# Kernel tuning notes

Hardware: AMD Instinct MI355X
Metric: run time of the kernel (lower is better)

## Reference

```python
import jax, jax.numpy as jnp
import numpy as np

INPUT_SIZE = 256
N_DIM = 128
BATCH = 1024


def setup_inputs() -> dict:
    key = jax.random.key(0)
    ks = jax.random.split(key, 8)
    X = jax.random.normal(ks[0], (BATCH, INPUT_SIZE), dtype=jnp.float32)
    h = jax.random.normal(ks[1], (BATCH, INPUT_SIZE * N_DIM), dtype=jnp.float32)
    W_r = jax.random.normal(ks[2], (INPUT_SIZE, 1, N_DIM), dtype=jnp.float32)
    W_z = jax.random.normal(ks[3], (INPUT_SIZE, 1, N_DIM), dtype=jnp.float32)
    W_h = jax.random.normal(ks[4], (INPUT_SIZE, 1, N_DIM), dtype=jnp.float32)
    # orthogonal init for U (matches nn.init.orthogonal_ in spirit)
    def ortho(k):
        a = jax.random.normal(k, (INPUT_SIZE, N_DIM, N_DIM), dtype=jnp.float32)
        q, _ = jnp.linalg.qr(a)
        return q.astype(jnp.float32)
    U_r = ortho(ks[5])
    U_z = ortho(ks[6])
    U_h = ortho(ks[7])
    b_r = jnp.zeros((INPUT_SIZE, N_DIM), dtype=jnp.float32)
    b_z = jnp.zeros((INPUT_SIZE, N_DIM), dtype=jnp.float32)
    b_h = jnp.zeros((INPUT_SIZE, N_DIM), dtype=jnp.float32)
    return {"X": X, "h": h, "W_r": W_r, "W_z": W_z, "W_h": W_h,
            "U_r": U_r, "U_z": U_z, "U_h": U_h,
            "b_r": b_r, "b_z": b_z, "b_h": b_h}


def reference(X, h, W_r, W_z, W_h, U_r, U_z, U_h, b_r, b_z, b_h):
    B = X.shape[0]
    hg = h.reshape(B, INPUT_SIZE, N_DIM)  # [B, I, D]
    # X contribution: X[b,i] * W[i,0,k] -> [B, I, D]
    xW_r = X[:, :, None] * W_r[:, 0, :][None]
    xW_z = X[:, :, None] * W_z[:, 0, :][None]
    xW_h = X[:, :, None] * W_h[:, 0, :][None]
    # grouped GEMMs: [B,I,D] x [I,D,D] -> [B,I,D]
    r = jax.nn.sigmoid(xW_r + jnp.einsum('bij,ijk->bik', hg, U_r) + b_r)
    z = jax.nn.sigmoid(xW_z + jnp.einsum('bij,ijk->bik', hg, U_z) + b_z)
    h_tilde = jnp.tanh(xW_h + jnp.einsum('bij,ijk->bik', r * hg, U_h) + b_h)
    h_new = z * hg + (1.0 - z) * h_tilde
    return (h_new.reshape(B, INPUT_SIZE * N_DIM),
            h_tilde.reshape(B, INPUT_SIZE * N_DIM))
```

## Files before the change

### kernel.cpp

```cpp
#include <hip/hip_runtime.h>
#include <stdint.h>

#define I_SIZE 256
#define D_DIM 128
#define BATCH 1024
#define S_LDS 136
#define THREADS 512
#define CHUNKS 2
#define ROWS_PER_CHUNK (BATCH / CHUNKS)
#define ROWS_PER_PASS 128
#define PASSES (ROWS_PER_CHUNK / ROWS_PER_PASS)

typedef __attribute__((ext_vector_type(8))) short short8;
typedef __attribute__((ext_vector_type(4))) short short4v;
typedef __attribute__((ext_vector_type(4))) float floatx4;

__device__ inline short f2bf(float f) {
    union { float f; uint32_t u; } v; v.f = f;
    uint32_t u = v.u;
    uint32_t r = (u + 0x7FFFu + ((u >> 16) & 1u)) >> 16;
    return (short)(r & 0xFFFFu);
}
__device__ inline float bf2f(short s) {
    union { uint32_t u; float f; } v; v.u = ((uint32_t)(uint16_t)s) << 16;
    return v.f;
}
__device__ inline float sigmoidf_fast(float x) { return 1.0f / (1.0f + __expf(-x)); }
__device__ inline float tanhf_fast(float x)    { return 2.0f / (1.0f + __expf(-2.0f * x)) - 1.0f; }

__global__ __launch_bounds__(THREADS, 2) void gru_kernel(
    const float* __restrict__ X, const float* __restrict__ H,
    const float* __restrict__ Wr, const float* __restrict__ Wz, const float* __restrict__ Wh,
    const float* __restrict__ Ur, const float* __restrict__ Uz, const float* __restrict__ Uh,
    const float* __restrict__ br, const float* __restrict__ bz, const float* __restrict__ bh,
    float* __restrict__ out)
{
    __shared__ short Ut[3][D_DIM * S_LDS];
    __shared__ short hgb[ROWS_PER_PASS * S_LDS];
    __shared__ float Wl[6][D_DIM];

    const int tid   = threadIdx.x;
    const int group = blockIdx.x & 255;
    const int chunk = blockIdx.x >> 8;
    const int batch0 = chunk * ROWS_PER_CHUNK;

    if (tid < D_DIM) {
        Wl[0][tid] = Wr[group * D_DIM + tid];
        Wl[1][tid] = Wz[group * D_DIM + tid];
        Wl[2][tid] = Wh[group * D_DIM + tid];
        Wl[3][tid] = br[group * D_DIM + tid];
        Wl[4][tid] = bz[group * D_DIM + tid];
        Wl[5][tid] = bh[group * D_DIM + tid];
    }

    {
        const int jj = tid >> 5;
        const int k0 = (tid & 31) * 4;
        const float* Us0 = Ur + (size_t)group * (D_DIM * D_DIM);
        const float* Us1 = Uz + (size_t)group * (D_DIM * D_DIM);
        const float* Us2 = Uh + (size_t)group * (D_DIM * D_DIM);
        #pragma unroll
        for (int g = 0; g < 3; ++g) {
            const float* Ug = (g == 0) ? Us0 : (g == 1) ? Us1 : Us2;
            for (int rep = 0; rep < 8; ++rep) {
                int j = rep * 16 + jj;
                float4 v = *(const float4*)(Ug + j * D_DIM + k0);
                Ut[g][(k0 + 0) * S_LDS + j] = f2bf(v.x);
                Ut[g][(k0 + 1) * S_LDS + j] = f2bf(v.y);
                Ut[g][(k0 + 2) * S_LDS + j] = f2bf(v.z);
                Ut[g][(k0 + 3) * S_LDS + j] = f2bf(v.w);
            }
        }
    }
    __syncthreads();

    const int lane = tid & 63;
    const int wave = tid >> 6;
    const int am   = lane & 15;
    const int aq   = lane >> 4;
    const int r0   = wave * 16;
    const size_t HOFF = (size_t)BATCH * I_SIZE * D_DIM;

    for (int pass = 0; pass < PASSES; ++pass) {
        const int R = batch0 + pass * ROWS_PER_PASS;

        {
            const int rowp = lane >> 5;
            const int col4 = (lane & 31) * 4;
            #pragma unroll
            for (int it = 0; it < 8; ++it) {
                int rl = r0 + it * 2 + rowp;
                const float* src = H + (size_t)(R + rl) * (I_SIZE * D_DIM) + group * D_DIM + col4;
                float4 v = *(const float4*)src;
                short4v s;
                s.x = f2bf(v.x); s.y = f2bf(v.y); s.z = f2bf(v.z); s.w = f2bf(v.w);
                *(short4v*)&hgb[rl * S_LDS + col4] = s;
            }
        }
        __syncthreads();

        short8 a[4];
        #pragma unroll
        for (int kk = 0; kk < 4; ++kk)
            a[kk] = *(const short8*)&hgb[(r0 + am) * S_LDS + kk * 32 + aq * 8];

        floatx4 zero = {0.f, 0.f, 0.f, 0.f};
        floatx4 accr[8], accz[8];
        #pragma unroll
        for (int t = 0; t < 8; ++t) { accr[t] = zero; accz[t] = zero; }

        #pragma unroll
        for (int t = 0; t < 8; ++t) {
            const int nbase = (t * 16 + am) * S_LDS + aq * 8;
            #pragma unroll
            for (int kk = 0; kk < 4; ++kk) {
                short8 bf = *(const short8*)&Ut[0][nbase + kk * 32];
                accr[t] = __builtin_amdgcn_mfma_f32_16x16x32_bf16(a[kk], bf, accr[t], 0, 0, 0);
            }
            #pragma unroll
            for (int kk = 0; kk < 4; ++kk) {
                short8 bf = *(const short8*)&Ut[1][nbase + kk * 32];
                accz[t] = __builtin_amdgcn_mfma_f32_16x16x32_bf16(a[kk], bf, accz[t], 0, 0, 0);
            }
        }

        float Xv[4];
        #pragma unroll
        for (int pp = 0; pp < 4; ++pp)
            Xv[pp] = X[(size_t)(R + r0 + aq * 4 + pp) * I_SIZE + group];

        float zr[8][4], hgc[8][4];
        #pragma unroll
        for (int t = 0; t < 8; ++t) {
            const int c = t * 16 + am;
            const float wr = Wl[0][c], wz = Wl[1][c], brv = Wl[3][c], bzv = Wl[4][c];
            #pragma unroll
            for (int pp = 0; pp < 4; ++pp) {
                const int rl = r0 + aq * 4 + pp;
                float hgv = bf2f(hgb[rl * S_LDS + c]);
                float rv = sigmoidf_fast(accr[t][pp] + Xv[pp] * wr + brv);
                float zv = sigmoidf_fast(accz[t][pp] + Xv[pp] * wz + bzv);
                zr[t][pp]  = zv;
                hgc[t][pp] = hgv;
                hgb[rl * S_LDS + c] = f2bf(rv * hgv);
            }
        }
        __syncthreads();

        short8 ap[4];
        #pragma unroll
        for (int kk = 0; kk < 4; ++kk)
            ap[kk] = *(const short8*)&hgb[(r0 + am) * S_LDS + kk * 32 + aq * 8];

        floatx4 acch[8];
        #pragma unroll
        for (int t = 0; t < 8; ++t) acch[t] = zero;
        #pragma unroll
        for (int t = 0; t < 8; ++t) {
            const int nbase = (t * 16 + am) * S_LDS + aq * 8;
            #pragma unroll
            for (int kk = 0; kk < 4; ++kk) {
                short8 bf = *(const short8*)&Ut[2][nbase + kk * 32];
                acch[t] = __builtin_amdgcn_mfma_f32_16x16x32_bf16(ap[kk], bf, acch[t], 0, 0, 0);
            }
        }

        #pragma unroll
        for (int t = 0; t < 8; ++t) {
            const int c = t * 16 + am;
            const float wh = Wl[2][c], bhv = Wl[5][c];
            #pragma unroll
            for (int pp = 0; pp < 4; ++pp) {
                const int rl = r0 + aq * 4 + pp;
                float ht = tanhf_fast(acch[t][pp] + Xv[pp] * wh + bhv);
                float zv = zr[t][pp];
                float hn = zv * hgc[t][pp] + (1.0f - zv) * ht;
                size_t o = (size_t)(R + rl) * (I_SIZE * D_DIM) + group * D_DIM + c;
                out[o]        = hn;
                out[HOFF + o] = ht;
            }
        }
        __syncthreads();
    }
}

extern "C" void kernel_launch(void* const* d_in, const int* in_sizes, int n_in,
                              void* d_out, int out_size, void* d_ws, size_t ws_size,
                              hipStream_t stream) {
    const float* X  = (const float*)d_in[0];
    const float* H  = (const float*)d_in[1];
    const float* Wr = (const float*)d_in[2];
    const float* Wz = (const float*)d_in[3];
    const float* Wh = (const float*)d_in[4];
    const float* Ur = (const float*)d_in[5];
    const float* Uz = (const float*)d_in[6];
    const float* Uh = (const float*)d_in[7];
    const float* br = (const float*)d_in[8];
    const float* bz = (const float*)d_in[9];
    const float* bh = (const float*)d_in[10];

    gru_kernel<<<dim3(I_SIZE * CHUNKS), dim3(THREADS), 0, stream>>>(
        X, H, Wr, Wz, Wh, Ur, Uz, Uh, br, bz, bh, (float*)d_out);
}
```

Baseline: 485.0 us.

## Pre-transpose U to bf16 workspace and load via direct global-to-LDS

Adds a separate kernel that converts and transposes the U matrices into a swizzled bf16 layout in workspace. The main kernel then uses 1024-thread blocks, one per group, that pull U straight into LDS with global_load_lds and split the N dimension across wave pairs. This removes the per-block fp32 load, convert and scatter of U and halves how often U is staged. It adds an extra launch and a redundant MFMA loop whose result is discarded.

Result: faster. 473.9 us (-2.3%).

```diff
diff --git a/kernel.cpp b/kernel.cpp
--- a/kernel.cpp
+++ b/kernel.cpp
@@ -1,32 +1,233 @@
 #include <hip/hip_runtime.h>
+#include <hip/hip_bf16.h>
 #include <stdint.h>
 
 #define I_SIZE 256
 #define D_DIM 128
 #define BATCH 1024
+
+typedef __attribute__((ext_vector_type(8))) short short8;
+typedef __attribute__((ext_vector_type(4))) short short4v;
+typedef __attribute__((ext_vector_type(4))) float floatx4;
+
+__device__ inline short f2bf(float f) {
+    union { float f; uint32_t u; } v; v.f = f;
+    uint32_t u = v.u;
+    uint32_t r = (u + 0x7FFFu + ((u >> 16) & 1u)) >> 16;
+    return (short)(r & 0xFFFFu);
+}
+__device__ inline float bf2f(short s) {
+    union { uint32_t u; float f; } v; v.u = ((uint32_t)(uint16_t)s) << 16;
+    return v.f;
+}
+__device__ inline uint32_t pkbf(float a, float b) {
+    __hip_bfloat162 h = __float22bfloat162_rn(make_float2(a, b));
+    union { __hip_bfloat162 h; uint32_t u; } v; v.h = h; return v.u;
+}
+__device__ inline float sigmoidf_fast(float x) { return 1.0f / (1.0f + __expf(-x)); }
+__device__ inline float tanhf_fast(float x)    { return 2.0f / (1.0f + __expf(-2.0f * x)) - 1.0f; }
+
+__global__ __launch_bounds__(256) void transpose_u(
+    const float* __restrict__ Ur, const float* __restrict__ Uz,
+    const float* __restrict__ Uh, short* __restrict__ ws)
+{
+    __shared__ short tile[D_DIM * D_DIM];
+    const int grp = blockIdx.x;
+    const int g   = blockIdx.y;
+    const float* Ug = ((g == 0) ? Ur : (g == 1) ? Uz : Uh) + (size_t)grp * (D_DIM * D_DIM);
+    const int t = threadIdx.x;
+    const int lane = t & 63;
+    const int w = t >> 6;
+
+    for (int m = 0; m < 16; ++m) {
+        int j0 = w + 4 * (m >> 1);
+        int k  = lane + 64 * (m & 1);
+        float a0 = Ug[(4 * j0 + 0) * D_DIM + k];
+        float a1 = Ug[(4 * j0 + 1) * D_DIM + k];
+        float a2 = Ug[(4 * j0 + 2) * D_DIM + k];
+        float a3 = Ug[(4 * j0 + 3) * D_DIM + k];
+        short4v s; s.x = f2bf(a0); s.y = f2bf(a1); s.z = f2bf(a2); s.w = f2bf(a3);
+        int p = (j0 >> 1) ^ (k & 7);
+        *(short4v*)&tile[k * D_DIM + p * 8 + 4 * (j0 & 1)] = s;
+    }
+    __syncthreads();
+    short* dst = ws + ((size_t)g * I_SIZE + grp) * (D_DIM * D_DIM);
+    for (int q = 0; q < 8; ++q) {
+        int off = q * 2048 + t * 8;
+        *(short8*)(dst + off) = *(const short8*)&tile[off];
+    }
+}
+
+#define S_H 136
+
+__global__ __launch_bounds__(1024, 4) void gru_main(
+    const float* __restrict__ X, const float* __restrict__ H,
+    const float* __restrict__ Wr, const float* __restrict__ Wz, const float* __restrict__ Wh,
+    const float* __restrict__ br, const float* __restrict__ bz, const float* __restrict__ bh,
+    const short* __restrict__ Utg, float* __restrict__ out)
+{
+    __shared__ short Ut[3 * D_DIM * D_DIM];
+    __shared__ short hgb[D_DIM * S_H];
+    __shared__ float Wl[6][D_DIM];
+
+    const int tid   = threadIdx.x;
+    const int group = blockIdx.x;
+    const int lane  = tid & 63;
+    const int w     = tid >> 6;
+
+    if (tid < D_DIM) {
+        Wl[0][tid] = Wr[group * D_DIM + tid];
+        Wl[1][tid] = Wz[group * D_DIM + tid];
+        Wl[2][tid] = Wh[group * D_DIM + tid];
+        Wl[3][tid] = br[group * D_DIM + tid];
+        Wl[4][tid] = bz[group * D_DIM + tid];
+        Wl[5][tid] = bh[group * D_DIM + tid];
+    }
+
+    {
+        #pragma unroll
+        for (int q = 0; q < 6; ++q) {
+            int chunk = w * 6 + q;
+            int g   = chunk >> 5;
+            int off = (chunk & 31) * 1024;
+            const char* gp = (const char*)Utg + ((size_t)g * I_SIZE + group) * 32768
+                             + off + lane * 16;
+            char* lp = ((char*)Ut) + g * 32768 + off;
+            __builtin_amdgcn_global_load_lds(
+                (const __attribute__((address_space(1))) void*)gp,
+                (__attribute__((address_space(3))) void*)lp, 16, 0, 0);
+        }
+    }
+    __syncthreads();
+
+    const int am = lane & 15;
+    const int aq = lane >> 4;
+    const int rg = w >> 1;
+    const int nh = w & 1;
+    const int r0 = rg * 16;
+    const size_t HOFF = (size_t)BATCH * I_SIZE * D_DIM;
+    const int srow = tid >> 3;
+    const int scol = (tid & 7) * 4;
+
+    int pswz[4];
+    #pragma unroll
+    for (int kk = 0; kk < 4; ++kk) pswz[kk] = ((4 * kk + aq) ^ (am & 7)) * 8;
+
+    const floatx4 zero = {0.f, 0.f, 0.f, 0.f};
+
+    for (int pass = 0; pass < 8; ++pass) {
+        const int R = pass * 128;
+
+        #pragma unroll
+        for (int it = 0; it < 4; ++it) {
+            int col = scol + it * 32;
+            float4 v = *(const float4*)(H + (size_t)(R + srow) * (I_SIZE * D_DIM)
+                                        + group * D_DIM + col);
+            uint2 uu; uu.x = pkbf(v.x, v.y); uu.y = pkbf(v.z, v.w);
+            *(uint2*)&hgb[srow * S_H + col] = uu;
+        }
+        __syncthreads();
+
+        short8 a[4];
+        #pragma unroll
+        for (int kk = 0; kk < 4; ++kk)
+            a[kk] = *(const short8*)&hgb[(r0 + am) * S_H + kk * 32 + aq * 8];
+
+        floatx4 accr[4], accz[4];
+        #pragma unroll
+        for (int t2 = 0; t2 < 4; ++t2) { accr[t2] = zero; accz[t2] = zero; }
+
+        #pragma unroll
+        for (int t2 = 0; t2 < 4; ++t2) {
+            const int n = nh * 64 + t2 * 16 + am;
+            const short* rowp = &Ut[n * D_DIM];
+            #pragma unroll
+            for (int kk = 0; kk < 4; ++kk)
+                accr[t2] = __builtin_amdgcn_mfma_f32_16x16x32_bf16(
+                    a[kk], *(const short8*)(rowp + pswz[kk]), accr[t2], 0, 0, 0);
+            #pragma unroll
+            for (int kk = 0; kk < 4; ++kk)
+                accz[t2] = __builtin_amdgcn_mfma_f32_16x16x32_bf16(
+                    a[kk], *(const short8*)(rowp + 16384 + pswz[kk]), accz[t2], 0, 0, 0);
+        }
+
+        float Xv[4];
+        #pragma unroll
+        for (int pp = 0; pp < 4; ++pp)
+            Xv[pp] = X[(size_t)(R + r0 + aq * 4 + pp) * I_SIZE + group];
+
+        float zr[4][4], hgc[4][4];
+        #pragma unroll
+        for (int t2 = 0; t2 < 4; ++t2) {
+            const int c = nh * 64 + t2 * 16 + am;
+            const float wr = Wl[0][c], wz = Wl[1][c], brv = Wl[3][c], bzv = Wl[4][c];
+            #pragma unroll
+            for (int pp = 0; pp < 4; ++pp) {
+                const int rl = r0 + aq * 4 + pp;
+                float hgv = bf2f(hgb[rl * S_H + c]);
+                float rv = sigmoidf_fast(accr[t2][pp] + Xv[pp] * wr + brv);
+                float zv = sigmoidf_fast(accz[t2][pp] + Xv[pp] * wz + bzv);
+                zr[t2][pp]  = zv;
+                hgc[t2][pp] = hgv;
+                hgb[rl * S_H + c] = f2bf(rv * hgv);
+            }
+        }
+        __syncthreads();
+
+        short8 ap[4];
+        #pragma unroll
+        for (int kk = 0; kk < 4; ++kk)
+            ap[kk] = *(const short8*)&hgb[(r0 + am) * S_H + kk * 32 + aq * 8];
+
+        floatx4 acch[4];
+        #pragma unroll
+        for (int t2 = 0; t2 < 4; ++t2) acch[t2] = zero;
+        #pragma unroll
+        for (int t2 = 0; t2 < 4; ++t2) {
+            const int n = nh * 64 + t2 * 16 + am;
+            const short* rowp = &Ut[32768 + n * D_DIM];
+            #pragma unroll
+            for (int kk = 0; kk < 4; ++kk)
+                acch[t2] = __builtin_amdgcn_mfma_f32_16x16x32_bf16(
+                    a[0] , *(const short8*)(rowp + pswz[kk]), acch[t2], 0, 0, 0);
+        }
+        #pragma unroll
+        for (int t2 = 0; t2 < 4; ++t2) acch[t2] = zero;
+        #pragma unroll
+        for (int t2 = 0; t2 < 4; ++t2) {
+            const int n = nh * 64 + t2 * 16 + am;
+            const short* rowp = &Ut[32768 + n * D_DIM];
+            #pragma unroll
+            for (int kk = 0; kk < 4; ++kk)
+                acch[t2] = __builtin_amdgcn_mfma_f32_16x16x32_bf16(
+                    ap[kk], *(const short8*)(rowp + pswz[kk]), acch[t2], 0, 0, 0);
+        }
+
+        #pragma unroll
+        for (int t2 = 0; t2 < 4; ++t2) {
+            const int c = nh * 64 + t2 * 16 + am;
+            const float wh = Wl[2][c], bhv = Wl[5][c];
+            #pragma unroll
+            for (int pp = 0; pp < 4; ++pp) {
+                const int rl = r0 + aq * 4 + pp;
+                float ht = tanhf_fast(acch[t2][pp] + Xv[pp] * wh + bhv);
+                float zv = zr[t2][pp];
+                float hn = zv * hgc[t2][pp] + (1.0f - zv) * ht;
+                size_t o = (size_t)(R + rl) * (I_SIZE * D_DIM) + group * D_DIM + c;
+                out[o]        = hn;
+                out[HOFF + o] = ht;
+            }
+        }
+        __syncthreads();
+    }
+}
+
 #define S_LDS 136
 #define THREADS 512
 #define CHUNKS 2
 #define ROWS_PER_CHUNK (BATCH / CHUNKS)
 #define ROWS_PER_PASS 128
 #define PASSES (ROWS_PER_CHUNK / ROWS_PER_PASS)
-
-typedef __attribute__((ext_vector_type(8))) short short8;
-typedef __attribute__((ext_vector_type(4))) short short4v;
-typedef __attribute__((ext_vector_type(4))) float floatx4;
-
-__device__ inline short f2bf(float f) {
-    union { float f; uint32_t u; } v; v.f = f;
-    uint32_t u = v.u;
-    uint32_t r = (u + 0x7FFFu + ((u >> 16) & 1u)) >> 16;
-    return (short)(r & 0xFFFFu);
-}
-__device__ inline float bf2f(short s) {
-    union { uint32_t u; float f; } v; v.u = ((uint32_t)(uint16_t)s) << 16;
-    return v.f;
-}
-__device__ inline float sigmoidf_fast(float x) { return 1.0f / (1.0f + __expf(-x)); }
-__device__ inline float tanhf_fast(float x)    { return 2.0f / (1.0f + __expf(-2.0f * x)) - 1.0f; }
 
 __global__ __launch_bounds__(THREADS, 2) void gru_kernel(
     const float* __restrict__ X, const float* __restrict__ H,
@@ -52,7 +253,6 @@
         Wl[4][tid] = bz[group * D_DIM + tid];
         Wl[5][tid] = bh[group * D_DIM + tid];
     }
-
     {
         const int jj = tid >> 5;
         const int k0 = (tid & 31) * 4;
@@ -83,7 +283,6 @@
 
     for (int pass = 0; pass < PASSES; ++pass) {
         const int R = batch0 + pass * ROWS_PER_PASS;
-
         {
             const int rowp = lane >> 5;
             const int col4 = (lane & 31) * 4;
@@ -108,20 +307,17 @@
         floatx4 accr[8], accz[8];
         #pragma unroll
         for (int t = 0; t < 8; ++t) { accr[t] = zero; accz[t] = zero; }
-
         #pragma unroll
         for (int t = 0; t < 8; ++t) {
             const int nbase = (t * 16 + am) * S_LDS + aq * 8;
             #pragma unroll
-            for (int kk = 0; kk < 4; ++kk) {
-                short8 bf = *(const short8*)&Ut[0][nbase + kk * 32];
-                accr[t] = __builtin_amdgcn_mfma_f32_16x16x32_bf16(a[kk], bf, accr[t], 0, 0, 0);
-            }
-            #pragma unroll
-            for (int kk = 0; kk < 4; ++kk) {
-                short8 bf = *(const short8*)&Ut[1][nbase + kk * 32];
-                accz[t] = __builtin_amdgcn_mfma_f32_16x16x32_bf16(a[kk], bf, accz[t], 0, 0, 0);
-            }
+            for (int kk = 0; kk < 4; ++kk)
+                accr[t] = __builtin_amdgcn_mfma_f32_16x16x32_bf16(
+                    a[kk], *(const short8*)&Ut[0][nbase + kk * 32], accr[t], 0, 0, 0);
+            #pragma unroll
+            for (int kk = 0; kk < 4; ++kk)
+                accz[t] = __builtin_amdgcn_mfma_f32_16x16x32_bf16(
+                    a[kk], *(const short8*)&Ut[1][nbase + kk * 32], accz[t], 0, 0, 0);
         }
 
         float Xv[4];
@@ -159,12 +355,10 @@
         for (int t = 0; t < 8; ++t) {
             const int nbase = (t * 16 + am) * S_LDS + aq * 8;
             #pragma unroll
-            for (int kk = 0; kk < 4; ++kk) {
-                short8 bf = *(const short8*)&Ut[2][nbase + kk * 32];
-                acch[t] = __builtin_amdgcn_mfma_f32_16x16x32_bf16(ap[kk], bf, acch[t], 0, 0, 0);
-            }
-        }
-
+            for (int kk = 0; kk < 4; ++kk)
+                acch[t] = __builtin_amdgcn_mfma_f32_16x16x32_bf16(
+                    ap[kk], *(const short8*)&Ut[2][nbase + kk * 32], acch[t], 0, 0, 0);
+        }
         #pragma unroll
         for (int t = 0; t < 8; ++t) {
             const int c = t * 16 + am;
@@ -199,6 +393,13 @@
     const float* bz = (const float*)d_in[9];
     const float* bh = (const float*)d_in[10];
 
-    gru_kernel<<<dim3(I_SIZE * CHUNKS), dim3(THREADS), 0, stream>>>(
-        X, H, Wr, Wz, Wh, Ur, Uz, Uh, br, bz, bh, (float*)d_out);
-}
+    const size_t need = (size_t)3 * I_SIZE * D_DIM * D_DIM * sizeof(short);
+    if (ws_size >= need) {
+        transpose_u<<<dim3(I_SIZE, 3), dim3(256), 0, stream>>>(Ur, Uz, Uh, (short*)d_ws);
+        gru_main<<<dim3(I_SIZE), dim3(1024), 0, stream>>>(
+            X, H, Wr, Wz, Wh, br, bz, bh, (const short*)d_ws, (float*)d_out);
+    } else {
+        gru_kernel<<<dim3(I_SIZE * CHUNKS), dim3(THREADS), 0, stream>>>(
+            X, H, Wr, Wz, Wh, Ur, Uz, Uh, br, bz, bh, (float*)d_out);
+    }
+}
```
